# Kernel optimization log

Measured on AMD Instinct MI355X. Metric: run time of the kernel, lower is better.

The kernel has to match this reference:

```python
import jax, jax.numpy as jnp
import numpy as np

LEAK = 0.01  # torch F.leaky_relu default slope


def _conv1d(x, W, b):
    # x: [B, Cin, L], W: [Cout, Cin, K] -> [B, Cout, L-K+1]
    y = jax.lax.conv_general_dilated(x, W, window_strides=(1,), padding='VALID',
                                     dimension_numbers=('NCH', 'OIH', 'NCH'))
    return y + b[None, :, None]


def _maxpool3(x):
    # MaxPool1d(kernel=3, stride=3, padding=1); torch pads with -inf
    return jax.lax.reduce_window(x, -jnp.inf, jax.lax.max,
                                 (1, 1, 3), (1, 1, 3),
                                 ((0, 0), (0, 0), (1, 1)))


def _lrelu(x):
    return jnp.where(x >= 0, x, LEAK * x)


def _lstm_layer(x, Wih, Whh, b):
    # x: [B, T, D]; Wih: [4H, D]; Whh: [4H, H]; b: [4H]  (torch gate order i,f,g,o)
    B = x.shape[0]
    H = Whh.shape[1]

    def step(carry, xt):
        h, c = carry
        gates = xt @ Wih.T + h @ Whh.T + b  # [B, 4H]
        i, f, g, o = jnp.split(gates, 4, axis=-1)
        c = jax.nn.sigmoid(f) * c + jax.nn.sigmoid(i) * jnp.tanh(g)
        h = jax.nn.sigmoid(o) * jnp.tanh(c)
        return (h, c), h

    init = (jnp.zeros((B, H), x.dtype), jnp.zeros((B, H), x.dtype))
    _, ys = jax.lax.scan(step, init, jnp.swapaxes(x, 0, 1))
    return jnp.swapaxes(ys, 0, 1)  # [B, T, H]


def _lstm3(x, Wih_s, Whh_s, b_s):
    # 3-layer LSTM (dropout=0 in eval); return h_n[-1] + h_n[-2]
    h_last = []
    for l in range(3):
        x = _lstm_layer(x, Wih_s[l], Whh_s[l], b_s[l])
        h_last.append(x[:, -1])
    return h_last[-1] + h_last[-2]


def _forward(data_in, W1, b1, W2, b2, W3, b3,
             fWih, fWhh, fb, tWih, tWhh, tb,
             L1W, L1b, L2W, L2b, L3W, L3b, L4W, L4b):
    T, F, L, P = data_in.shape
    x = data_in.reshape(T * F, L, P).swapaxes(1, 2)  # [B, 3, L]
    x = _maxpool3(_lrelu(_conv1d(x, W1, b1)))  # [B, 10, 170]
    x = _maxpool3(_lrelu(_conv1d(x, W2, b2)))  # [B, 5, 56]
    x = _maxpool3(_lrelu(_conv1d(x, W3, b3)))  # [B, 10, 18]
    x = x.swapaxes(1, 2)                       # [B, 18, 10] packet vectors
    fv = _lstm3(x, fWih, fWhh, fb)             # [B, 10] flow vectors
    fv = fv.reshape(T, F, -1)                  # [T, F, 10]
    tv = _lstm3(fv, tWih, tWhh, tb)            # [T, 10] trace vectors
    h = _lrelu(tv @ L1W.T + L1b)
    h = _lrelu(h @ L2W.T + L2b)
    h = _lrelu(h @ L3W.T + L3b)
    return h @ L4W.T + L4b                     # [T, 7]


def setup_inputs() -> dict:
    key = jax.random.key(0)
    ks = iter(jax.random.split(key, 32))
    n = lambda shape: jax.random.normal(next(ks), shape, dtype=jnp.float32)
    return {
        'data_in': n((64, 64, 512, 3)),
        'W1': n((10, 3, 5)), 'b1': n((10,)),
        'W2': n((5, 10, 5)), 'b2': n((5,)),
        'W3': n((10, 5, 5)), 'b3': n((10,)),
        'fWih': n((3, 40, 10)), 'fWhh': n((3, 40, 10)), 'fb': n((3, 40)),
        'tWih': n((3, 40, 10)), 'tWhh': n((3, 40, 10)), 'tb': n((3, 40)),
        'L1W': n((128, 10)), 'L1b': n((128,)),
        'L2W': n((256, 128)), 'L2b': n((256,)),
        'L3W': n((64, 256)), 'L3b': n((64,)),
        'L4W': n((7, 64)), 'L4b': n((7,)),
    }


def reference(data_in, W1, b1, W2, b2, W3, b3,
              fWih, fWhh, fb, tWih, tWhh, tb,
              L1W, L1b, L2W, L2b, L3W, L3b, L4W, L4b):
    return _forward(data_in, W1, b1, W2, b2, W3, b3,
                    fWih, fWhh, fb, tWih, tWhh, tb,
                    L1W, L1b, L2W, L2b, L3W, L3b, L4W, L4b)
```

## Files before the change

kernel.cpp:

```cpp
#include <hip/hip_runtime.h>
#include <math.h>

#define LEAK 0.01f

typedef float v2f __attribute__((ext_vector_type(2)));

#define PIN(x) asm("" : "+v"(x))

__device__ __forceinline__ float lrelu(float x) { return fmaxf(x, LEAK * x); }
__device__ __forceinline__ float fast_rcp(float x) { return __builtin_amdgcn_rcpf(x); }
__device__ __forceinline__ float sigmoid_f(float x) {
    return fast_rcp(1.0f + exp2f(-1.44269504f * x));
}
__device__ __forceinline__ float tanh_f(float x) {
    return 2.0f * fast_rcp(1.0f + exp2f(-2.88539008f * x)) - 1.0f;
}
__device__ __forceinline__ float readlane_f(float v, int l) {
    return __int_as_float(__builtin_amdgcn_readlane(__float_as_int(v), l));
}

#define DECL5(p) v2f p##_0, p##_1, p##_2, p##_3, p##_4
#define LOAD5(p, src) do { const v2f* _s5 = (const v2f*)(src); \
    p##_0 = _s5[0]; p##_1 = _s5[1]; p##_2 = _s5[2]; p##_3 = _s5[3]; p##_4 = _s5[4]; } while (0)
#define CP5(d, s) do { d##_0 = s##_0; d##_1 = s##_1; d##_2 = s##_2; d##_3 = s##_3; d##_4 = s##_4; } while (0)
#define ZERO5(p) do { p##_0 = (v2f){0.f,0.f}; p##_1 = (v2f){0.f,0.f}; p##_2 = (v2f){0.f,0.f}; \
    p##_3 = (v2f){0.f,0.f}; p##_4 = (v2f){0.f,0.f}; } while (0)
#define DOT5(w, x) ((w##_0 * x##_0 + w##_1 * x##_1) + (w##_2 * x##_2 + w##_3 * x##_3) + w##_4 * x##_4)

#define DECLU(u) float u##0, u##1, u##2, u##3, u##4, u##5, u##6, u##7, u##8, u##9
#define ZEROU(u) do { u##0=u##1=u##2=u##3=u##4=u##5=u##6=u##7=u##8=u##9=0.0f; } while (0)
#define DOTU(w, u) (fmaf(w##_0.x, u##0, fmaf(w##_0.y, u##1, fmaf(w##_1.x, u##2, fmaf(w##_1.y, u##3, w##_2.x * u##4)))) \
                  + fmaf(w##_2.y, u##5, fmaf(w##_3.x, u##6, fmaf(w##_3.y, u##7, fmaf(w##_4.x, u##8, w##_4.y * u##9)))))

#define DECLW(p) v2f p##0, p##1, p##2, p##3, p##4, p##5, p##6, p##7, p##8, p##9
#define LOADW_PAIR(p, q0, q1) do { \
    p##0 = (v2f){(q0)[0], (q1)[0]}; p##1 = (v2f){(q0)[1], (q1)[1]}; \
    p##2 = (v2f){(q0)[2], (q1)[2]}; p##3 = (v2f){(q0)[3], (q1)[3]}; \
    p##4 = (v2f){(q0)[4], (q1)[4]}; p##5 = (v2f){(q0)[5], (q1)[5]}; \
    p##6 = (v2f){(q0)[6], (q1)[6]}; p##7 = (v2f){(q0)[7], (q1)[7]}; \
    p##8 = (v2f){(q0)[8], (q1)[8]}; p##9 = (v2f){(q0)[9], (q1)[9]}; } while (0)
#define PINW(p) do { PIN(p##0); PIN(p##1); PIN(p##2); PIN(p##3); PIN(p##4); \
    PIN(p##5); PIN(p##6); PIN(p##7); PIN(p##8); PIN(p##9); } while (0)
#define PKDOT(acc, w, s) do { \
    acc += w##0 * (v2f){s##0, s##0}; acc += w##1 * (v2f){s##1, s##1}; \
    acc += w##2 * (v2f){s##2, s##2}; acc += w##3 * (v2f){s##3, s##3}; \
    acc += w##4 * (v2f){s##4, s##4}; acc += w##5 * (v2f){s##5, s##5}; \
    acc += w##6 * (v2f){s##6, s##6}; acc += w##7 * (v2f){s##7, s##7}; \
    acc += w##8 * (v2f){s##8, s##8}; acc += w##9 * (v2f){s##9, s##9}; } while (0)

#define L1C 508
#define L1P 170
#define L2C 166
#define L2P 56
#define L3C 52
#define L3P 18
#define TT 18

__global__ __launch_bounds__(256, 4) void conv_kernel(
    const float* __restrict__ in,
    const float* __restrict__ W1, const float* __restrict__ b1,
    const float* __restrict__ W2, const float* __restrict__ b2,
    const float* __restrict__ W3, const float* __restrict__ b3,
    float* __restrict__ xseq)
{
    __shared__ __align__(16) float xsraw[24 + 1536 + 24];
    __shared__ __align__(16) float y1raw[16 + L1P * 10 + 32];
    __shared__ __align__(16) float y2raw[8 + L2P * 6 + 24];
    float* xs = xsraw + 24;
    float* y1 = y1raw + 16;
    float* y2 = y2raw + 8;

    const int tid = threadIdx.x;
    const int b = blockIdx.x;

    {
        const float4* src = (const float4*)(in + (size_t)b * 1536);
        float4* dst4 = (float4*)xs;
        for (int i = tid; i < 384; i += 256) dst4[i] = src[i];
    }
    __syncthreads();

    {
        const int co = tid % 10;
        const int ob = tid / 10;
        if (tid < 250) {
            float w[15];
            #pragma unroll
            for (int q = 0; q < 15; ++q) w[q] = W1[co * 15 + q];
            const float bias = b1[co];
            const int o0 = ob * 7;
            int sb = 3 * o0 - 1;
            float win[21];
            #pragma unroll
            for (int q = 0; q < 21; ++q) win[q] = xs[3 * sb + q];
            #pragma unroll
            for (int r = 0; r < 7; ++r) {
                const int o = o0 + r;
                if (o < L1P) {
                    float a0 = bias, a1 = bias, a2 = bias;
                    #pragma unroll
                    for (int p = 0; p < 3; ++p) {
                        #pragma unroll
                        for (int k = 0; k < 5; ++k) {
                            const float wv = w[p * 5 + k];
                            a0 = fmaf(wv, win[3 * k + p], a0);
                            a1 = fmaf(wv, win[3 * (k + 1) + p], a1);
                            a2 = fmaf(wv, win[3 * (k + 2) + p], a2);
                        }
                    }
                    float best = -3.0e38f;
                    if (sb >= 0)        best = fmaxf(best, lrelu(a0));
                    best = fmaxf(best, lrelu(a1));
                    if (sb + 2 < L1C)   best = fmaxf(best, lrelu(a2));
                    y1[o * 10 + co] = best;
                }
                if (r < 6 && o + 1 < L1P) {
                    #pragma unroll
                    for (int q = 0; q < 12; ++q) win[q] = win[q + 9];
                    #pragma unroll
                    for (int q = 0; q < 9; ++q) win[12 + q] = xs[3 * sb + 21 + q];
                    sb += 3;
                }
            }
        }
    }
    __syncthreads();

    {
        const int co = tid % 5;
        const int ob = tid / 5;
        v2f wv2[25];
        #pragma unroll
        for (int c2 = 0; c2 < 5; ++c2)
            #pragma unroll
            for (int k = 0; k < 5; ++k)
                wv2[c2 * 5 + k] = (v2f){W2[co * 50 + (2 * c2) * 5 + k],
                                        W2[co * 50 + (2 * c2 + 1) * 5 + k]};
        const float bias = b2[co];
        if (tid < 255) {
            for (int r = 0; r < 2; ++r) {
                const int o = ob + 51 * r;
                if (o < L2P) {
                    const int t0 = 3 * o - 1;
                    v2f v0 = {0.f, 0.f}, v1 = {0.f, 0.f}, v2 = {0.f, 0.f};
                    #pragma unroll
                    for (int m = 0; m < 7; ++m) {
                        v2f rows5[5];
                        const v2f* pr = (const v2f*)(y1 + (t0 + m) * 10);
                        #pragma unroll
                        for (int c2 = 0; c2 < 5; ++c2) rows5[c2] = pr[c2];
                        #pragma unroll
                        for (int c2 = 0; c2 < 5; ++c2) {
                            if (m < 5)            v0 += wv2[c2 * 5 + m] * rows5[c2];
                            if (m >= 1 && m <= 5) v1 += wv2[c2 * 5 + m - 1] * rows5[c2];
                            if (m >= 2)           v2 += wv2[c2 * 5 + m - 2] * rows5[c2];
                        }
                    }
                    const float a0 = bias + v0.x + v0.y;
                    const float a1 = bias + v1.x + v1.y;
                    const float a2 = bias + v2.x + v2.y;
                    float best = -3.0e38f;
                    if (t0 >= 0)        best = fmaxf(best, lrelu(a0));
                    best = fmaxf(best, lrelu(a1));
                    if (t0 + 2 < L2C)   best = fmaxf(best, lrelu(a2));
                    y2[o * 6 + co] = best;
                }
            }
        }
    }
    __syncthreads();

    {
        const int co = tid % 10;
        const int o = tid / 10;
        if (o < L3P) {
            v2f wv3[10];
            float ws3[5];
            #pragma unroll
            for (int c2 = 0; c2 < 2; ++c2)
                #pragma unroll
                for (int k = 0; k < 5; ++k)
                    wv3[c2 * 5 + k] = (v2f){W3[co * 25 + (2 * c2) * 5 + k],
                                            W3[co * 25 + (2 * c2 + 1) * 5 + k]};
            #pragma unroll
            for (int k = 0; k < 5; ++k) ws3[k] = W3[co * 25 + 20 + k];
            const float bias = b3[co];
            const int t0 = 3 * o - 1;
            v2f v0 = {0.f, 0.f}, v1 = {0.f, 0.f}, v2 = {0.f, 0.f};
            float s0 = 0.f, s1 = 0.f, s2 = 0.f;
            #pragma unroll
            for (int m = 0; m < 7; ++m) {
                const float* base = y2 + (t0 + m) * 6;
                v2f ra0 = ((const v2f*)base)[0];
                v2f ra1 = ((const v2f*)base)[1];
                float rcm = base[4];
                if (m < 5) {
                    v0 += wv3[m] * ra0; v0 += wv3[5 + m] * ra1;
                    s0 = fmaf(ws3[m], rcm, s0);
                }
                if (m >= 1 && m <= 5) {
                    v1 += wv3[m - 1] * ra0; v1 += wv3[5 + m - 1] * ra1;
                    s1 = fmaf(ws3[m - 1], rcm, s1);
                }
                if (m >= 2) {
                    v2 += wv3[m - 2] * ra0; v2 += wv3[5 + m - 2] * ra1;
                    s2 = fmaf(ws3[m - 2], rcm, s2);
                }
            }
            const float a0 = bias + s0 + v0.x + v0.y;
            const float a1 = bias + s1 + v1.x + v1.y;
            const float a2 = bias + s2 + v2.x + v2.y;
            float best = -3.0e38f;
            if (t0 >= 0)        best = fmaxf(best, lrelu(a0));
            best = fmaxf(best, lrelu(a1));
            if (t0 + 2 < L3C)   best = fmaxf(best, lrelu(a2));
            xseq[(size_t)b * 180 + o * 10 + co] = best;
        }
    }
}

__global__ __launch_bounds__(256) __attribute__((amdgpu_waves_per_eu(1, 1)))
void flow_lstm_kernel(
    const float* __restrict__ xseq,
    const float* __restrict__ fWih, const float* __restrict__ fWhh,
    const float* __restrict__ fb,
    float* __restrict__ fv)
{
    __shared__ __align__(16) float sbuf[3][16 * 18 * 10];
    const int tid = threadIdx.x;
    const int blk = blockIdx.x;

    {
        const float* src = xseq + (size_t)blk * 2880;
        for (int i = tid; i < 2880; i += 256) sbuf[0][i] = src[i];
    }
    __syncthreads();

    const int el = tid >> 4;
    const int j = tid & 15;
    const int jj = (j < 10) ? j : 0;
    const int base = el * 180;
    const int lane = tid & 63;
    const int gbase = lane & 48;

    float fv_acc = 0.0f;

    for (int l = 0; l < 3; ++l) {
        const float* Wi = fWih + l * 400;
        const float* Wh = fWhh + l * 400;
        const float* bb = fb + l * 40;
        DECL5(wii); DECL5(wif); DECL5(wig); DECL5(wio);
        DECL5(whi); DECL5(whf); DECL5(whg); DECL5(who);
        LOAD5(wii, Wi + jj * 10);
        LOAD5(wif, Wi + (10 + jj) * 10);
        LOAD5(wig, Wi + (20 + jj) * 10);
        LOAD5(wio, Wi + (30 + jj) * 10);
        LOAD5(whi, Wh + jj * 10);
        LOAD5(whf, Wh + (10 + jj) * 10);
        LOAD5(whg, Wh + (20 + jj) * 10);
        LOAD5(who, Wh + (30 + jj) * 10);
        const float bi = bb[jj], bf = bb[10 + jj], bg = bb[20 + jj], bo = bb[30 + jj];

        const float* inb = sbuf[l];
        float* outb = sbuf[(l + 1) % 3];
        float c = 0.0f, hj = 0.0f;
        DECL5(hv); ZERO5(hv);
        DECL5(xc); DECL5(xn);
        LOAD5(xc, inb + base);

        for (int t = 0; t < TT; ++t) {
            if (t + 1 < TT) LOAD5(xn, inb + base + (t + 1) * 10);
            v2f ti_ = DOT5(wii, xc) + DOT5(whi, hv);
            v2f tf_ = DOT5(wif, xc) + DOT5(whf, hv);
            v2f tg_ = DOT5(wig, xc) + DOT5(whg, hv);
            v2f to_ = DOT5(wio, xc) + DOT5(who, hv);
            const float ai = sigmoid_f(bi + ti_.x + ti_.y);
            const float af = sigmoid_f(bf + tf_.x + tf_.y);
            const float ag = tanh_f(bg + tg_.x + tg_.y);
            const float ao = sigmoid_f(bo + to_.x + to_.y);
            c = af * c + ai * ag;
            hj = ao * tanh_f(c);
            if (j < 10) outb[base + t * 10 + j] = hj;
            hv_0 = (v2f){__shfl(hj, gbase + 0), __shfl(hj, gbase + 1)};
            hv_1 = (v2f){__shfl(hj, gbase + 2), __shfl(hj, gbase + 3)};
            hv_2 = (v2f){__shfl(hj, gbase + 4), __shfl(hj, gbase + 5)};
            hv_3 = (v2f){__shfl(hj, gbase + 6), __shfl(hj, gbase + 7)};
            hv_4 = (v2f){__shfl(hj, gbase + 8), __shfl(hj, gbase + 9)};
            CP5(xc, xn);
        }
        if (l >= 1) fv_acc += hj;
        __asm__ __volatile__("" ::: "memory");
    }
    if (j < 10) fv[(size_t)(blk * 16 + el) * 10 + j] = fv_acc;
}

__global__ __launch_bounds__(64) __attribute__((amdgpu_waves_per_eu(1, 1)))
void trace_mlp_kernel(
    const float* __restrict__ fv,
    const float* __restrict__ tWih, const float* __restrict__ tWhh,
    const float* __restrict__ tb,
    const float* __restrict__ L1W, const float* __restrict__ L1b,
    const float* __restrict__ L2W, const float* __restrict__ L2b,
    const float* __restrict__ L3W, const float* __restrict__ L3b,
    const float* __restrict__ L4W, const float* __restrict__ L4b,
    float* __restrict__ out)
{
    __shared__ __align__(16) float xrow[640];
    __shared__ __align__(16) float m1[128];
    __shared__ __align__(16) float m2b[256];
    __shared__ __align__(16) float m3[64];

    const int lane = threadIdx.x;
    const int ti = blockIdx.x;

    {
        const float4* src = (const float4*)(fv + (size_t)ti * 640);
        float4* dst = (float4*)xrow;
        for (int i = lane; i < 160; i += 64) dst[i] = src[i];
    }
    __asm__ __volatile__("" ::: "memory");

    const int g = (lane < 30) ? (lane / 10) : 2;
    const int j = lane % 10;

    const float* WiL = tWih + g * 400;
    const float* WhL = tWhh + g * 400;
    const float* bL  = tb + g * 40;
    DECLW(wxA); DECLW(wxB); DECLW(whA); DECLW(whB);
    LOADW_PAIR(wxA, WiL + j * 10,        WiL + (10 + j) * 10);
    LOADW_PAIR(wxB, WiL + (20 + j) * 10, WiL + (30 + j) * 10);
    LOADW_PAIR(whA, WhL + j * 10,        WhL + (10 + j) * 10);
    LOADW_PAIR(whB, WhL + (20 + j) * 10, WhL + (30 + j) * 10);
    v2f bA = (v2f){bL[j], bL[10 + j]};
    v2f bB = (v2f){bL[20 + j], bL[30 + j]};
    PINW(wxA); PINW(wxB); PINW(whA); PINW(whB);
    PIN(bA); PIN(bB);

    DECLU(u0); DECLU(u1); DECLU(u2);
    ZEROU(u0); ZEROU(u1); ZEROU(u2);
    float c = 0.0f, h = 0.0f;
    const int tlo = g, thi = 63 + g;
    const bool g0 = (g == 0), g1 = (g == 1);

    DECL5(xc); DECL5(xn);
    LOAD5(xc, xrow);

    for (int tau = 0; tau < 66; ++tau) {
        const int tn = (tau + 1 < 64) ? (tau + 1) : 63;
        LOAD5(xn, xrow + tn * 10);

        const float in0 = g0 ? xc_0.x : (g1 ? u00 : u10);
        const float in1 = g0 ? xc_0.y : (g1 ? u01 : u11);
        const float in2 = g0 ? xc_1.x : (g1 ? u02 : u12);
        const float in3 = g0 ? xc_1.y : (g1 ? u03 : u13);
        const float in4 = g0 ? xc_2.x : (g1 ? u04 : u14);
        const float in5 = g0 ? xc_2.y : (g1 ? u05 : u15);
        const float in6 = g0 ? xc_3.x : (g1 ? u06 : u16);
        const float in7 = g0 ? xc_3.y : (g1 ? u07 : u17);
        const float in8 = g0 ? xc_4.x : (g1 ? u08 : u18);
        const float in9 = g0 ? xc_4.y : (g1 ? u09 : u19);
        const float hd0 = g0 ? u00 : (g1 ? u10 : u20);
        const float hd1 = g0 ? u01 : (g1 ? u11 : u21);
        const float hd2 = g0 ? u02 : (g1 ? u12 : u22);
        const float hd3 = g0 ? u03 : (g1 ? u13 : u23);
        const float hd4 = g0 ? u04 : (g1 ? u14 : u24);
        const float hd5 = g0 ? u05 : (g1 ? u15 : u25);
        const float hd6 = g0 ? u06 : (g1 ? u16 : u26);
        const float hd7 = g0 ? u07 : (g1 ? u17 : u27);
        const float hd8 = g0 ? u08 : (g1 ? u18 : u28);
        const float hd9 = g0 ? u09 : (g1 ? u19 : u29);

        v2f gA = bA, gB = bB;
        PKDOT(gA, wxA, in); PKDOT(gB, wxB, in);
        PKDOT(gA, whA, hd); PKDOT(gB, whB, hd);

        const float ai = sigmoid_f(gA.x);
        const float af = sigmoid_f(gA.y);
        const float ag = tanh_f(gB.x);
        const float ao = sigmoid_f(gB.y);
        const float cn = af * c + ai * ag;
        const float hn = ao * tanh_f(cn);
        const bool act = (tau >= tlo) && (tau <= thi);
        c = act ? cn : c;
        h = act ? hn : h;

        u00 = readlane_f(h, 0); u01 = readlane_f(h, 1); u02 = readlane_f(h, 2);
        u03 = readlane_f(h, 3); u04 = readlane_f(h, 4); u05 = readlane_f(h, 5);
        u06 = readlane_f(h, 6); u07 = readlane_f(h, 7); u08 = readlane_f(h, 8);
        u09 = readlane_f(h, 9);
        u10 = readlane_f(h, 10); u11 = readlane_f(h, 11); u12 = readlane_f(h, 12);
        u13 = readlane_f(h, 13); u14 = readlane_f(h, 14); u15 = readlane_f(h, 15);
        u16 = readlane_f(h, 16); u17 = readlane_f(h, 17); u18 = readlane_f(h, 18);
        u19 = readlane_f(h, 19);
        u20 = readlane_f(h, 20); u21 = readlane_f(h, 21); u22 = readlane_f(h, 22);
        u23 = readlane_f(h, 23); u24 = readlane_f(h, 24); u25 = readlane_f(h, 25);
        u26 = readlane_f(h, 26); u27 = readlane_f(h, 27); u28 = readlane_f(h, 28);
        u29 = readlane_f(h, 29);

        CP5(xc, xn);
    }

    DECLU(tv);
    tv0 = u10 + u20; tv1 = u11 + u21; tv2 = u12 + u22; tv3 = u13 + u23;
    tv4 = u14 + u24; tv5 = u15 + u25; tv6 = u16 + u26; tv7 = u17 + u27;
    tv8 = u18 + u28; tv9 = u19 + u29;

    {
        DECL5(w1a); DECL5(w1b);
        LOAD5(w1a, L1W + lane * 10);
        LOAD5(w1b, L1W + (lane + 64) * 10);
        float a0 = L1b[lane] + DOTU(w1a, tv);
        float a1 = L1b[lane + 64] + DOTU(w1b, tv);
        m1[lane] = lrelu(a0);
        m1[lane + 64] = lrelu(a1);
    }
    __asm__ __volatile__("" ::: "memory");
    {
        float acc0 = L2b[lane];
        float acc1 = L2b[lane + 64];
        float acc2 = L2b[lane + 128];
        float acc3 = L2b[lane + 192];
        for (int k = 0; k < 128; k += 4) {
            float4 hv = *(const float4*)(m1 + k);
            float4 w0 = *(const float4*)(L2W + (size_t)lane * 128 + k);
            float4 w1 = *(const float4*)(L2W + (size_t)(lane + 64) * 128 + k);
            float4 w2 = *(const float4*)(L2W + (size_t)(lane + 128) * 128 + k);
            float4 w3 = *(const float4*)(L2W + (size_t)(lane + 192) * 128 + k);
            acc0 = fmaf(w0.x, hv.x, acc0); acc0 = fmaf(w0.y, hv.y, acc0);
            acc0 = fmaf(w0.z, hv.z, acc0); acc0 = fmaf(w0.w, hv.w, acc0);
            acc1 = fmaf(w1.x, hv.x, acc1); acc1 = fmaf(w1.y, hv.y, acc1);
            acc1 = fmaf(w1.z, hv.z, acc1); acc1 = fmaf(w1.w, hv.w, acc1);
            acc2 = fmaf(w2.x, hv.x, acc2); acc2 = fmaf(w2.y, hv.y, acc2);
            acc2 = fmaf(w2.z, hv.z, acc2); acc2 = fmaf(w2.w, hv.w, acc2);
            acc3 = fmaf(w3.x, hv.x, acc3); acc3 = fmaf(w3.y, hv.y, acc3);
            acc3 = fmaf(w3.z, hv.z, acc3); acc3 = fmaf(w3.w, hv.w, acc3);
        }
        m2b[lane] = lrelu(acc0);
        m2b[lane + 64] = lrelu(acc1);
        m2b[lane + 128] = lrelu(acc2);
        m2b[lane + 192] = lrelu(acc3);
    }
    __asm__ __volatile__("" ::: "memory");
    {
        float acc = L3b[lane];
        for (int k = 0; k < 256; k += 4) {
            float4 hv = *(const float4*)(m2b + k);
            float4 wv = *(const float4*)(L3W + (size_t)lane * 256 + k);
            acc = fmaf(wv.x, hv.x, acc);
            acc = fmaf(wv.y, hv.y, acc);
            acc = fmaf(wv.z, hv.z, acc);
            acc = fmaf(wv.w, hv.w, acc);
        }
        m3[lane] = lrelu(acc);
    }
    __asm__ __volatile__("" ::: "memory");
    if (lane < 7) {
        float acc = L4b[lane];
        #pragma unroll
        for (int k = 0; k < 64; k += 4) {
            float4 hv = *(const float4*)(m3 + k);
            float4 wv = *(const float4*)(L4W + lane * 64 + k);
            acc = fmaf(wv.x, hv.x, acc);
            acc = fmaf(wv.y, hv.y, acc);
            acc = fmaf(wv.z, hv.z, acc);
            acc = fmaf(wv.w, hv.w, acc);
        }
        out[ti * 7 + lane] = acc;
    }
}

extern "C" void kernel_launch(void* const* d_in, const int* in_sizes, int n_in,
                              void* d_out, int out_size, void* d_ws, size_t ws_size,
                              hipStream_t stream)
{
    const float* data_in = (const float*)d_in[0];
    const float* W1 = (const float*)d_in[1];
    const float* b1 = (const float*)d_in[2];
    const float* W2 = (const float*)d_in[3];
    const float* b2 = (const float*)d_in[4];
    const float* W3 = (const float*)d_in[5];
    const float* b3 = (const float*)d_in[6];
    const float* fWih = (const float*)d_in[7];
    const float* fWhh = (const float*)d_in[8];
    const float* fb = (const float*)d_in[9];
    const float* tWih = (const float*)d_in[10];
    const float* tWhh = (const float*)d_in[11];
    const float* tb = (const float*)d_in[12];
    const float* L1W = (const float*)d_in[13];
    const float* L1b = (const float*)d_in[14];
    const float* L2W = (const float*)d_in[15];
    const float* L2b = (const float*)d_in[16];
    const float* L3W = (const float*)d_in[17];
    const float* L3b = (const float*)d_in[18];
    const float* L4W = (const float*)d_in[19];
    const float* L4b = (const float*)d_in[20];

    float* xseq = (float*)d_ws;
    float* fv = xseq + 4096 * 180;
    float* outp = (float*)d_out;

    conv_kernel<<<4096, 256, 0, stream>>>(data_in, W1, b1, W2, b2, W3, b3, xseq);
    flow_lstm_kernel<<<256, 256, 0, stream>>>(xseq, fWih, fWhh, fb, fv);
    trace_mlp_kernel<<<64, 64, 0, stream>>>(fv, tWih, tWhh, tb,
                                            L1W, L1b, L2W, L2b, L3W, L3b,
                                            L4W, L4b, outp);
}
```

Measured before the change: 198.0 us.

## Use ds_bpermute for trace-LSTM state exchange and keep inputs in registers

The trace LSTM kernel now holds each timestep's input row in registers of a matching lane and fetches it with readlane, instead of staging it in shared memory. Per-layer hidden inputs are gathered with ds_bpermute using lane-dependent indices. This replaces 30 uniform readlanes plus 20 three-way selects per step with 20 bpermutes. The gate dot products are also split into four independent accumulator chains to shorten the dependency chain. The cost is that bpermute goes through LDS hardware and has longer latency than readlane, which may slow the serial recurrence.

```diff
diff --git a/kernel.cpp b/kernel.cpp
--- a/kernel.cpp
+++ b/kernel.cpp
@@ -17,6 +17,9 @@
 }
 __device__ __forceinline__ float readlane_f(float v, int l) {
     return __int_as_float(__builtin_amdgcn_readlane(__float_as_int(v), l));
+}
+__device__ __forceinline__ float bperm_f(int byte_idx, float v) {
+    return __int_as_float(__builtin_amdgcn_ds_bpermute(byte_idx, __float_as_int(v)));
 }
 
 #define DECL5(p) v2f p##_0, p##_1, p##_2, p##_3, p##_4
@@ -28,7 +31,6 @@
 #define DOT5(w, x) ((w##_0 * x##_0 + w##_1 * x##_1) + (w##_2 * x##_2 + w##_3 * x##_3) + w##_4 * x##_4)
 
 #define DECLU(u) float u##0, u##1, u##2, u##3, u##4, u##5, u##6, u##7, u##8, u##9
-#define ZEROU(u) do { u##0=u##1=u##2=u##3=u##4=u##5=u##6=u##7=u##8=u##9=0.0f; } while (0)
 #define DOTU(w, u) (fmaf(w##_0.x, u##0, fmaf(w##_0.y, u##1, fmaf(w##_1.x, u##2, fmaf(w##_1.y, u##3, w##_2.x * u##4)))) \
                   + fmaf(w##_2.y, u##5, fmaf(w##_3.x, u##6, fmaf(w##_3.y, u##7, fmaf(w##_4.x, u##8, w##_4.y * u##9)))))
 
@@ -41,12 +43,23 @@
     p##8 = (v2f){(q0)[8], (q1)[8]}; p##9 = (v2f){(q0)[9], (q1)[9]}; } while (0)
 #define PINW(p) do { PIN(p##0); PIN(p##1); PIN(p##2); PIN(p##3); PIN(p##4); \
     PIN(p##5); PIN(p##6); PIN(p##7); PIN(p##8); PIN(p##9); } while (0)
-#define PKDOT(acc, w, s) do { \
-    acc += w##0 * (v2f){s##0, s##0}; acc += w##1 * (v2f){s##1, s##1}; \
-    acc += w##2 * (v2f){s##2, s##2}; acc += w##3 * (v2f){s##3, s##3}; \
-    acc += w##4 * (v2f){s##4, s##4}; acc += w##5 * (v2f){s##5, s##5}; \
-    acc += w##6 * (v2f){s##6, s##6}; acc += w##7 * (v2f){s##7, s##7}; \
-    acc += w##8 * (v2f){s##8, s##8}; acc += w##9 * (v2f){s##9, s##9}; } while (0)
+
+#define SP(x) ((v2f){(x), (x)})
+#define GATES(gRes, wx, wh, bias) \
+    v2f gRes; { \
+        v2f q0 = bias; \
+        q0 += wx##0 * SP(IN0); q0 += wx##2 * SP(IN2); q0 += wx##4 * SP(IN4); \
+        q0 += wx##6 * SP(IN6); q0 += wx##8 * SP(IN8); \
+        v2f q1 = wx##1 * SP(IN1); \
+        q1 += wx##3 * SP(IN3); q1 += wx##5 * SP(IN5); \
+        q1 += wx##7 * SP(IN7); q1 += wx##9 * SP(IN9); \
+        v2f q2 = wh##0 * SP(HD0); \
+        q2 += wh##2 * SP(HD2); q2 += wh##4 * SP(HD4); \
+        q2 += wh##6 * SP(HD6); q2 += wh##8 * SP(HD8); \
+        v2f q3 = wh##1 * SP(HD1); \
+        q3 += wh##3 * SP(HD3); q3 += wh##5 * SP(HD5); \
+        q3 += wh##7 * SP(HD7); q3 += wh##9 * SP(HD9); \
+        gRes = (q0 + q1) + (q2 + q3); }
 
 #define L1C 508
 #define L1P 170
@@ -305,23 +318,25 @@
     const float* __restrict__ L4W, const float* __restrict__ L4b,
     float* __restrict__ out)
 {
-    __shared__ __align__(16) float xrow[640];
     __shared__ __align__(16) float m1[128];
     __shared__ __align__(16) float m2b[256];
     __shared__ __align__(16) float m3[64];
 
     const int lane = threadIdx.x;
     const int ti = blockIdx.x;
-
-    {
-        const float4* src = (const float4*)(fv + (size_t)ti * 640);
-        float4* dst = (float4*)xrow;
-        for (int i = lane; i < 160; i += 64) dst[i] = src[i];
-    }
-    __asm__ __volatile__("" ::: "memory");
-
     const int g = (lane < 30) ? (lane / 10) : 2;
     const int j = lane % 10;
+    const bool isL0 = (lane < 10);
+
+    float xr0, xr1, xr2, xr3, xr4, xr5, xr6, xr7, xr8, xr9;
+    {
+        const float2* xp = (const float2*)(fv + (size_t)ti * 640 + lane * 10);
+        float2 v0 = xp[0], v1 = xp[1], v2 = xp[2], v3 = xp[3], v4 = xp[4];
+        xr0 = v0.x; xr1 = v0.y; xr2 = v1.x; xr3 = v1.y; xr4 = v2.x;
+        xr5 = v2.y; xr6 = v3.x; xr7 = v3.y; xr8 = v4.x; xr9 = v4.y;
+    }
+    PIN(xr0); PIN(xr1); PIN(xr2); PIN(xr3); PIN(xr4);
+    PIN(xr5); PIN(xr6); PIN(xr7); PIN(xr8); PIN(xr9);
 
     const float* WiL = tWih + g * 400;
     const float* WhL = tWhh + g * 400;
@@ -336,43 +351,38 @@
     PINW(wxA); PINW(wxB); PINW(whA); PINW(whB);
     PIN(bA); PIN(bB);
 
-    DECLU(u0); DECLU(u1); DECLU(u2);
-    ZEROU(u0); ZEROU(u1); ZEROU(u2);
+    const int idx_hd = g * 40;
+    const int idx_in = (g == 0) ? 0 : (g - 1) * 40;
+
+    float HD0 = 0.f, HD1 = 0.f, HD2 = 0.f, HD3 = 0.f, HD4 = 0.f;
+    float HD5 = 0.f, HD6 = 0.f, HD7 = 0.f, HD8 = 0.f, HD9 = 0.f;
+    float IN0 = isL0 ? readlane_f(xr0, 0) : 0.f;
+    float IN1 = isL0 ? readlane_f(xr1, 0) : 0.f;
+    float IN2 = isL0 ? readlane_f(xr2, 0) : 0.f;
+    float IN3 = isL0 ? readlane_f(xr3, 0) : 0.f;
+    float IN4 = isL0 ? readlane_f(xr4, 0) : 0.f;
+    float IN5 = isL0 ? readlane_f(xr5, 0) : 0.f;
+    float IN6 = isL0 ? readlane_f(xr6, 0) : 0.f;
+    float IN7 = isL0 ? readlane_f(xr7, 0) : 0.f;
+    float IN8 = isL0 ? readlane_f(xr8, 0) : 0.f;
+    float IN9 = isL0 ? readlane_f(xr9, 0) : 0.f;
     float c = 0.0f, h = 0.0f;
-    const int tlo = g, thi = 63 + g;
-    const bool g0 = (g == 0), g1 = (g == 1);
-
-    DECL5(xc); DECL5(xn);
-    LOAD5(xc, xrow);
 
     for (int tau = 0; tau < 66; ++tau) {
         const int tn = (tau + 1 < 64) ? (tau + 1) : 63;
-        LOAD5(xn, xrow + tn * 10);
-
-        const float in0 = g0 ? xc_0.x : (g1 ? u00 : u10);
-        const float in1 = g0 ? xc_0.y : (g1 ? u01 : u11);
-        const float in2 = g0 ? xc_1.x : (g1 ? u02 : u12);
-        const float in3 = g0 ? xc_1.y : (g1 ? u03 : u13);
-        const float in4 = g0 ? xc_2.x : (g1 ? u04 : u14);
-        const float in5 = g0 ? xc_2.y : (g1 ? u05 : u15);
-        const float in6 = g0 ? xc_3.x : (g1 ? u06 : u16);
-        const float in7 = g0 ? xc_3.y : (g1 ? u07 : u17);
-        const float in8 = g0 ? xc_4.x : (g1 ? u08 : u18);
-        const float in9 = g0 ? xc_4.y : (g1 ? u09 : u19);
-        const float hd0 = g0 ? u00 : (g1 ? u10 : u20);
-        const float hd1 = g0 ? u01 : (g1 ? u11 : u21);
-        const float hd2 = g0 ? u02 : (g1 ? u12 : u22);
-        const float hd3 = g0 ? u03 : (g1 ? u13 : u23);
-        const float hd4 = g0 ? u04 : (g1 ? u14 : u24);
-        const float hd5 = g0 ? u05 : (g1 ? u15 : u25);
-        const float hd6 = g0 ? u06 : (g1 ? u16 : u26);
-        const float hd7 = g0 ? u07 : (g1 ? u17 : u27);
-        const float hd8 = g0 ? u08 : (g1 ? u18 : u28);
-        const float hd9 = g0 ? u09 : (g1 ? u19 : u29);
-
-        v2f gA = bA, gB = bB;
-        PKDOT(gA, wxA, in); PKDOT(gB, wxB, in);
-        PKDOT(gA, whA, hd); PKDOT(gB, whB, hd);
+        const float nx0 = readlane_f(xr0, tn);
+        const float nx1 = readlane_f(xr1, tn);
+        const float nx2 = readlane_f(xr2, tn);
+        const float nx3 = readlane_f(xr3, tn);
+        const float nx4 = readlane_f(xr4, tn);
+        const float nx5 = readlane_f(xr5, tn);
+        const float nx6 = readlane_f(xr6, tn);
+        const float nx7 = readlane_f(xr7, tn);
+        const float nx8 = readlane_f(xr8, tn);
+        const float nx9 = readlane_f(xr9, tn);
+
+        GATES(gA, wxA, whA, bA);
+        GATES(gB, wxB, whB, bB);
 
         const float ai = sigmoid_f(gA.x);
         const float af = sigmoid_f(gA.y);
@@ -380,30 +390,53 @@
         const float ao = sigmoid_f(gB.y);
         const float cn = af * c + ai * ag;
         const float hn = ao * tanh_f(cn);
-        const bool act = (tau >= tlo) && (tau <= thi);
+        const bool act = (tau >= g) && (tau - g <= 63);
         c = act ? cn : c;
         h = act ? hn : h;
 
-        u00 = readlane_f(h, 0); u01 = readlane_f(h, 1); u02 = readlane_f(h, 2);
-        u03 = readlane_f(h, 3); u04 = readlane_f(h, 4); u05 = readlane_f(h, 5);
-        u06 = readlane_f(h, 6); u07 = readlane_f(h, 7); u08 = readlane_f(h, 8);
-        u09 = readlane_f(h, 9);
-        u10 = readlane_f(h, 10); u11 = readlane_f(h, 11); u12 = readlane_f(h, 12);
-        u13 = readlane_f(h, 13); u14 = readlane_f(h, 14); u15 = readlane_f(h, 15);
-        u16 = readlane_f(h, 16); u17 = readlane_f(h, 17); u18 = readlane_f(h, 18);
-        u19 = readlane_f(h, 19);
-        u20 = readlane_f(h, 20); u21 = readlane_f(h, 21); u22 = readlane_f(h, 22);
-        u23 = readlane_f(h, 23); u24 = readlane_f(h, 24); u25 = readlane_f(h, 25);
-        u26 = readlane_f(h, 26); u27 = readlane_f(h, 27); u28 = readlane_f(h, 28);
-        u29 = readlane_f(h, 29);
-
-        CP5(xc, xn);
+        HD0 = bperm_f(idx_hd + 0,  h);
+        HD1 = bperm_f(idx_hd + 4,  h);
+        HD2 = bperm_f(idx_hd + 8,  h);
+        HD3 = bperm_f(idx_hd + 12, h);
+        HD4 = bperm_f(idx_hd + 16, h);
+        HD5 = bperm_f(idx_hd + 20, h);
+        HD6 = bperm_f(idx_hd + 24, h);
+        HD7 = bperm_f(idx_hd + 28, h);
+        HD8 = bperm_f(idx_hd + 32, h);
+        HD9 = bperm_f(idx_hd + 36, h);
+        const float i0 = bperm_f(idx_in + 0,  h);
+        const float i1 = bperm_f(idx_in + 4,  h);
+        const float i2 = bperm_f(idx_in + 8,  h);
+        const float i3 = bperm_f(idx_in + 12, h);
+        const float i4 = bperm_f(idx_in + 16, h);
+        const float i5 = bperm_f(idx_in + 20, h);
+        const float i6 = bperm_f(idx_in + 24, h);
+        const float i7 = bperm_f(idx_in + 28, h);
+        const float i8 = bperm_f(idx_in + 32, h);
+        const float i9 = bperm_f(idx_in + 36, h);
+        IN0 = isL0 ? nx0 : i0;
+        IN1 = isL0 ? nx1 : i1;
+        IN2 = isL0 ? nx2 : i2;
+        IN3 = isL0 ? nx3 : i3;
+        IN4 = isL0 ? nx4 : i4;
+        IN5 = isL0 ? nx5 : i5;
+        IN6 = isL0 ? nx6 : i6;
+        IN7 = isL0 ? nx7 : i7;
+        IN8 = isL0 ? nx8 : i8;
+        IN9 = isL0 ? nx9 : i9;
     }
 
     DECLU(tv);
-    tv0 = u10 + u20; tv1 = u11 + u21; tv2 = u12 + u22; tv3 = u13 + u23;
-    tv4 = u14 + u24; tv5 = u15 + u25; tv6 = u16 + u26; tv7 = u17 + u27;
-    tv8 = u18 + u28; tv9 = u19 + u29;
+    tv0 = readlane_f(h, 10) + readlane_f(h, 20);
+    tv1 = readlane_f(h, 11) + readlane_f(h, 21);
+    tv2 = readlane_f(h, 12) + readlane_f(h, 22);
+    tv3 = readlane_f(h, 13) + readlane_f(h, 23);
+    tv4 = readlane_f(h, 14) + readlane_f(h, 24);
+    tv5 = readlane_f(h, 15) + readlane_f(h, 25);
+    tv6 = readlane_f(h, 16) + readlane_f(h, 26);
+    tv7 = readlane_f(h, 17) + readlane_f(h, 27);
+    tv8 = readlane_f(h, 18) + readlane_f(h, 28);
+    tv9 = readlane_f(h, 19) + readlane_f(h, 29);
 
     {
         DECL5(w1a); DECL5(w1b);
```

Result: no change. 196.5 us (-0.7%).
